# Performance work log

Hardware: AMD Instinct MI355X
Metric: run time of the kernel (lower is better)

Reference implementation:

```python
import jax, jax.numpy as jnp
import numpy as np

N_POINTS = 10000
N_SHAPES = 100
N_RAYS = 4096
SH_COEFFS = 16  # (sh_degree+1)^2, degree 3


def sh_basis(d):
    """Degree-3 real SH basis. d: [B,3] normalized dirs -> [B,16]."""
    x, y, z = d[:, 0], d[:, 1], d[:, 2]
    one = jnp.ones_like(x)
    return jnp.stack([
        0.282095 * one,
        0.488603 * y, 0.488603 * z, 0.488603 * x,
        1.092548 * x * y, 1.092548 * y * z, 0.315392 * (3.0 * z * z - 1.0),
        1.092548 * x * z, 0.546274 * (x * x - y * y),
        0.590044 * y * (3.0 * x * x - y * y), 2.890611 * x * y * z,
        0.457046 * y * (5.0 * z * z - 1.0), 0.373176 * z * (5.0 * z * z - 3.0),
        0.457046 * x * (5.0 * z * z - 1.0), 1.445306 * z * (x * x - y * y),
        0.590044 * x * (x * x - 3.0 * y * y),
    ], axis=-1)


def setup_inputs() -> dict:
    key = jax.random.key(0)
    ks = jax.random.split(key, 7)
    return {
        "rays_o": jax.random.normal(ks[0], (N_RAYS, 3), jnp.float32),
        "rays_d": jax.random.normal(ks[1], (N_RAYS, 3), jnp.float32),
        "positions": jax.random.normal(ks[2], (N_POINTS, 3), jnp.float32),
        "shape_indices": jax.random.randint(ks[3], (N_POINTS,), 0, N_SHAPES, jnp.int32),
        "log_delta": jax.random.normal(ks[4], (N_SHAPES,), jnp.float32) * 0.1 - 1.0,
        "log_sigma": jax.random.normal(ks[5], (N_SHAPES,), jnp.float32) * 0.1,
        "raw_opacity": jax.random.uniform(ks[6], (N_POINTS,), jnp.float32, -0.1, 0.1),
        "sh_coeffs": jax.random.normal(jax.random.fold_in(key, 7), (N_POINTS, SH_COEFFS, 3), jnp.float32) * 0.1,
    }


def reference(rays_o, rays_d, positions, shape_indices, log_delta, log_sigma, raw_opacity, sh_coeffs):
    # normalize view directions (F.normalize)
    d_norm = rays_d / jnp.linalg.norm(rays_d, axis=-1, keepdims=True)

    opacity = jax.nn.sigmoid(raw_opacity)           # [N]
    point_delta = jnp.exp(log_delta)[shape_indices]  # [N]
    point_sigma = jnp.exp(log_sigma)[shape_indices]  # [N]

    # SH shading: colors [N, B, 3]
    sh = sh_basis(d_norm)                            # [B, 16]
    colors = jax.nn.sigmoid(jnp.einsum('nkc,bk->nbc', sh_coeffs, sh))

    # per point / per ray geometry
    rel = positions[:, None, :] - rays_o[None, :, :]   # [N, B, 3]
    dist = jnp.linalg.norm(rel, axis=2)                # [N, B]
    dirs = rel / (dist[..., None] + 1e-8)              # [N, B, 3]
    dot = jnp.sum(dirs * d_norm[None, :, :], axis=2)   # [N, B]

    contrib = (jnp.exp(-point_delta[:, None] * (1.0 - dot) ** 2)
               * point_sigma[:, None] * opacity[:, None] / (dist + 1e-6))  # [N, B]
    total = jnp.sum(contrib, axis=0, keepdims=True)
    w = contrib / (total + 1e-8)                       # [N, B]

    rgb = jnp.sum(colors * w[..., None], axis=0)       # [B, 3]
    depth = jnp.sum(dist * w, axis=0)[:, None]         # [B, 1]
    opac = jnp.broadcast_to(jnp.mean(opacity), (rgb.shape[0],))
    return rgb, depth, opac
```

## Files before the change

### kernel.cpp

```cpp
#include <hip/hip_runtime.h>
#include <hip/hip_bf16.h>

#define NPTS    10000
#define NRAYS   4096
#define PTILES  640
#define RTILES  256
#define RGROUPS 64
#define PCHUNKS 16
#define TPC     (PTILES / PCHUNKS)
#define ABLK    64
#define BBLK    160
#define LOG2E   1.44269504f

typedef float f4  __attribute__((ext_vector_type(4)));
typedef short s8v __attribute__((ext_vector_type(8)));

__device__ s8v   g_A[RTILES * 4 * 64];
__device__ s8v   g_B[PTILES * 7 * 64];
__device__ float g_acc[NRAYS * 5];
__device__ float g_oppart[BBLK];

__device__ __forceinline__ float fast_rcp(float x)  { return __builtin_amdgcn_rcpf(x); }
__device__ __forceinline__ float fast_exp2(float x) { return __builtin_amdgcn_exp2f(x); }
__device__ __forceinline__ float fast_sigmoid(float x) { return fast_rcp(1.0f + fast_exp2(-x * LOG2E)); }

__device__ __forceinline__ unsigned short bf16r(float x) {
    __hip_bfloat16 h = __float2bfloat16(x);
    return *reinterpret_cast<unsigned short*>(&h);
}
__device__ __forceinline__ float bf16f(unsigned short u) {
    return __uint_as_float((unsigned)u << 16);
}
__device__ __forceinline__ float bfhi(float x) { return bf16f(bf16r(x)); }

__device__ __forceinline__ s8v pk8(float a, float b, float c, float d,
                                   float e, float f, float g, float h) {
    s8v r;
    r[0] = (short)bf16r(a); r[1] = (short)bf16r(b);
    r[2] = (short)bf16r(c); r[3] = (short)bf16r(d);
    r[4] = (short)bf16r(e); r[5] = (short)bf16r(f);
    r[6] = (short)bf16r(g); r[7] = (short)bf16r(h);
    return r;
}

template <int CTRL>
__device__ __forceinline__ float dpp_step(float x) {
    return x + __int_as_float(
        __builtin_amdgcn_update_dpp(0, __float_as_int(x), CTRL, 0xf, 0xf, true));
}
__device__ __forceinline__ float rowsum15(float x) {
    x = dpp_step<0x111>(x);
    x = dpp_step<0x112>(x);
    x = dpp_step<0x114>(x);
    x = dpp_step<0x118>(x);
    return x;
}

__global__ __launch_bounds__(256) void setup(const float* __restrict__ ro,
                                             const float* __restrict__ rd,
                                             const float* __restrict__ pos,
                                             const int*   __restrict__ sidx,
                                             const float* __restrict__ log_delta,
                                             const float* __restrict__ log_sigma,
                                             const float* __restrict__ raw_op,
                                             const float* __restrict__ shc) {
    s8v zero8 = pk8(0, 0, 0, 0, 0, 0, 0, 0);
    if (blockIdx.x < ABLK) {
        int t = blockIdx.x * 256 + threadIdx.x;
        int rt = t >> 6, lane = t & 63, quad = lane >> 4;
        int r = rt * 16 + (lane & 15);
        if (quad == 0) {
            float* a = g_acc + (size_t)r * 5;
            a[0] = a[1] = a[2] = a[3] = a[4] = 0.0f;
        }
        float ox = ro[r * 3 + 0], oy = ro[r * 3 + 1], oz = ro[r * 3 + 2];
        float rdx = rd[r * 3 + 0], rdy = rd[r * 3 + 1], rdz = rd[r * 3 + 2];
        float inv = __builtin_amdgcn_rsqf(rdx * rdx + rdy * rdy + rdz * rdz);
        float x = rdx * inv, y = rdy * inv, z = rdz * inv;
        float oo = ox * ox + oy * oy + oz * oz;
        float od = ox * x + oy * y + oz * z;
        float ohx = bfhi(ox), olx = ox - ohx;
        float ohy = bfhi(oy), oly = oy - ohy;
        float ohz = bfhi(oz), olz = oz - ohz;
        float dhx = bfhi(x),  dlx = x - dhx;
        float dhy = bfhi(y),  dly = y - dhy;
        float dhz = bfhi(z),  dlz = z - dhz;
        float ooh = bfhi(oo), ool = oo - ooh;
        float odh = bfhi(od), odl = od - odh;
        float zz = z * z, xx = x * x, yy = y * y;
        float sh[16];
        sh[0]  = LOG2E * 0.282095f;
        sh[1]  = LOG2E * 0.488603f * y;
        sh[2]  = LOG2E * 0.488603f * z;
        sh[3]  = LOG2E * 0.488603f * x;
        sh[4]  = LOG2E * 1.092548f * x * y;
        sh[5]  = LOG2E * 1.092548f * y * z;
        sh[6]  = LOG2E * 0.315392f * (3.0f * zz - 1.0f);
        sh[7]  = LOG2E * 1.092548f * x * z;
        sh[8]  = LOG2E * 0.546274f * (xx - yy);
        sh[9]  = LOG2E * 0.590044f * y * (3.0f * xx - yy);
        sh[10] = LOG2E * 2.890611f * x * y * z;
        sh[11] = LOG2E * 0.457046f * y * (5.0f * zz - 1.0f);
        sh[12] = LOG2E * 0.373176f * z * (5.0f * zz - 3.0f);
        sh[13] = LOG2E * 0.457046f * x * (5.0f * zz - 1.0f);
        sh[14] = LOG2E * 1.445306f * z * (xx - yy);
        sh[15] = LOG2E * 0.590044f * x * (xx - 3.0f * yy);

        s8v A0 = quad == 0 ? pk8(1, 1, ooh, ool, ohx, ohy, ohz, ohx)
               : quad == 1 ? pk8(ohy, ohz, olx, oly, olz, 0, 0, 0) : zero8;
        s8v A1 = quad == 0 ? pk8(dhx, dhy, dhz, dhx, dhy, dhz, dlx, dly)
               : quad == 1 ? pk8(dlz, odh, odl, 0, 0, 0, 0, 0) : zero8;
        s8v A2 = quad == 0 ? pk8(sh[0], sh[1], sh[2], sh[3], sh[4], sh[5], sh[6], sh[7])
               : quad == 1 ? pk8(sh[8], sh[9], sh[10], sh[11], sh[12], sh[13], sh[14], sh[15]) : zero8;
        s8v A3 = quad == 0 ? pk8(1, 1, 0, 0, 0, 0, 0, 0) : zero8;
        s8v* pa = g_A + (size_t)rt * 4 * 64 + lane;
        pa[0 * 64] = A0; pa[1 * 64] = A1; pa[2 * 64] = A2; pa[3 * 64] = A3;
    } else {
        int bb = blockIdx.x - ABLK;
        int t  = bb * 256 + threadIdx.x;
        int pt = t >> 6, lane = t & 63, quad = lane >> 4;
        int n  = pt * 16 + (lane & 15);
        float px, py, pz, w1, L0, op = 0.0f;
        float C0[16], C1[16], C2[16];
        if (n < NPTS) {
            px = pos[n * 3 + 0]; py = pos[n * 3 + 1]; pz = pos[n * 3 + 2];
            int s = sidx[n];
            op = fast_sigmoid(raw_op[n]);
            w1 = -__expf(log_delta[s]) * LOG2E;
            float w0 = __expf(log_sigma[s]) * op;
            L0 = __log2f(w0);
            const float* c = shc + (size_t)n * 48;
#pragma unroll
            for (int k = 0; k < 16; ++k) {
                C0[k] = c[k * 3 + 0]; C1[k] = c[k * 3 + 1]; C2[k] = c[k * 3 + 2];
            }
        } else {
            px = py = pz = 1e3f; w1 = 0.0f; L0 = -100.0f;
#pragma unroll
            for (int k = 0; k < 16; ++k) { C0[k] = 0; C1[k] = 0; C2[k] = 0; }
        }
        float pp  = px * px + py * py + pz * pz;
        float phx = bfhi(px), plx = px - phx;
        float phy = bfhi(py), ply = py - phy;
        float phz = bfhi(pz), plz = pz - phz;
        float pph = bfhi(pp), ppl = pp - pph;
        float w1h = bfhi(w1), w1l = w1 - w1h;
        float L0h = bfhi(L0), L0l = L0 - L0h;

        s8v B0 = quad == 0 ? pk8(pph, ppl, 1, 1, -2 * phx, -2 * phy, -2 * phz, -2 * plx)
               : quad == 1 ? pk8(-2 * ply, -2 * plz, -2 * phx, -2 * phy, -2 * phz, 0, 0, 0) : zero8;
        s8v B1 = quad == 0 ? pk8(phx, phy, phz, plx, ply, plz, phx, phy)
               : quad == 1 ? pk8(phz, -1, -1, 0, 0, 0, 0, 0) : zero8;
        s8v B2 = quad == 0 ? pk8(C0[0], C0[1], C0[2], C0[3], C0[4], C0[5], C0[6], C0[7])
               : quad == 1 ? pk8(C0[8], C0[9], C0[10], C0[11], C0[12], C0[13], C0[14], C0[15]) : zero8;
        s8v B3 = quad == 0 ? pk8(C1[0], C1[1], C1[2], C1[3], C1[4], C1[5], C1[6], C1[7])
               : quad == 1 ? pk8(C1[8], C1[9], C1[10], C1[11], C1[12], C1[13], C1[14], C1[15]) : zero8;
        s8v B4 = quad == 0 ? pk8(C2[0], C2[1], C2[2], C2[3], C2[4], C2[5], C2[6], C2[7])
               : quad == 1 ? pk8(C2[8], C2[9], C2[10], C2[11], C2[12], C2[13], C2[14], C2[15]) : zero8;
        s8v B5 = quad == 0 ? pk8(w1h, w1l, 0, 0, 0, 0, 0, 0) : zero8;
        s8v B6 = quad == 0 ? pk8(L0h, L0l, 0, 0, 0, 0, 0, 0) : zero8;
        s8v* pb = g_B + (size_t)pt * 7 * 64 + lane;
        pb[0 * 64] = B0; pb[1 * 64] = B1; pb[2 * 64] = B2; pb[3 * 64] = B3;
        pb[4 * 64] = B4; pb[5 * 64] = B5; pb[6 * 64] = B6;

        __shared__ float blk;
        if (threadIdx.x == 0) blk = 0.0f;
        __syncthreads();
        float v = (quad == 0) ? op : 0.0f;
#pragma unroll
        for (int off = 32; off > 0; off >>= 1) v += __shfl_down(v, off, 64);
        if ((threadIdx.x & 63) == 0) atomicAdd(&blk, v);
        __syncthreads();
        if (threadIdx.x == 0) g_oppart[bb] = blk;
    }
}

__global__ __launch_bounds__(256, 3) void nerf_main() {
    int rg = blockIdx.x & (RGROUPS - 1);
    int pc = blockIdx.x / RGROUPS;
    int wv = threadIdx.x >> 6, lane = threadIdx.x & 63;
    int rt = rg * 4 + wv;

    const s8v* pa = g_A + (size_t)rt * 4 * 64 + lane;
    s8v a0 = pa[0 * 64], a1 = pa[1 * 64], a2 = pa[2 * 64], a3 = pa[3 * 64];
    f4 z = {0.0f, 0.0f, 0.0f, 0.0f};

    float acc[5][4];
#pragma unroll
    for (int v = 0; v < 5; ++v)
#pragma unroll
        for (int i = 0; i < 4; ++i) acc[v][i] = 0.0f;

    const s8v* pb = g_B + (size_t)(pc * TPC) * 7 * 64 + lane;
#pragma unroll 1
    for (int ti = 0; ti < TPC; ++ti, pb += 7 * 64) {
        s8v b0 = pb[0 * 64], b1 = pb[1 * 64], b2 = pb[2 * 64], b3 = pb[3 * 64];
        s8v b4 = pb[4 * 64], b5 = pb[5 * 64], b6 = pb[6 * 64];
        f4 c0 = __builtin_amdgcn_mfma_f32_16x16x32_bf16(a0, b0, z, 0, 0, 0);
        f4 c1 = __builtin_amdgcn_mfma_f32_16x16x32_bf16(a1, b1, z, 0, 0, 0);
        f4 c2 = __builtin_amdgcn_mfma_f32_16x16x32_bf16(a2, b2, z, 0, 0, 0);
        f4 c3 = __builtin_amdgcn_mfma_f32_16x16x32_bf16(a2, b3, z, 0, 0, 0);
        f4 c4 = __builtin_amdgcn_mfma_f32_16x16x32_bf16(a2, b4, z, 0, 0, 0);
        f4 c5 = __builtin_amdgcn_mfma_f32_16x16x32_bf16(a3, b5, z, 0, 0, 0);
        f4 c6 = __builtin_amdgcn_mfma_f32_16x16x32_bf16(a3, b6, z, 0, 0, 0);
#pragma unroll
        for (int i = 0; i < 4; ++i) {
            float d2  = c0[i], pd = c1[i];
            float inv = __builtin_amdgcn_rsqf(d2);
            float t   = 1.0f - pd * inv;
            float arg = fmaf(c5[i] * t, t, c6[i]);
            float contrib = fast_exp2(arg) * inv;
            float dist = d2 * inv;
            float e0 = 1.0f + fast_exp2(-c2[i]);
            float e1 = 1.0f + fast_exp2(-c3[i]);
            float e2 = 1.0f + fast_exp2(-c4[i]);
            float P  = e0 * e1, Pa = P * e2;
            float CI = contrib * fast_rcp(Pa);
            acc[0][i] = fmaf(CI, e1 * e2, acc[0][i]);
            acc[1][i] = fmaf(CI, e0 * e2, acc[1][i]);
            acc[2][i] = fmaf(CI, P, acc[2][i]);
            acc[3][i] = fmaf(dist, contrib, acc[3][i]);
            acc[4][i] += contrib;
        }
    }

#pragma unroll
    for (int v = 0; v < 5; ++v)
#pragma unroll
        for (int i = 0; i < 4; ++i) acc[v][i] = rowsum15(acc[v][i]);
    if ((lane & 15) == 15) {
        int quad = lane >> 4;
#pragma unroll
        for (int i = 0; i < 4; ++i) {
            float* ac = g_acc + (size_t)(rt * 16 + quad * 4 + i) * 5;
            atomicAdd(ac + 0, acc[0][i]);
            atomicAdd(ac + 1, acc[1][i]);
            atomicAdd(ac + 2, acc[2][i]);
            atomicAdd(ac + 3, acc[3][i]);
            atomicAdd(ac + 4, acc[4][i]);
        }
    }
}

__global__ void finalize(float* __restrict__ out) {
    int r = blockIdx.x * blockDim.x + threadIdx.x;
    if (r >= NRAYS) return;
    float opv = 0.0f;
    for (int i = 0; i < BBLK; ++i) opv += g_oppart[i];
    const float* a = g_acc + (size_t)r * 5;
    float inv = fast_rcp(a[4] + 1e-8f);
    out[r * 3 + 0]     = a[0] * inv;
    out[r * 3 + 1]     = a[1] * inv;
    out[r * 3 + 2]     = a[2] * inv;
    out[NRAYS * 3 + r] = a[3] * inv;
    out[NRAYS * 4 + r] = opv * (1.0f / NPTS);
}

extern "C" void kernel_launch(void* const* d_in, const int* in_sizes, int n_in,
                              void* d_out, int out_size, void* d_ws, size_t ws_size,
                              hipStream_t stream) {
    const float* rays_o    = (const float*)d_in[0];
    const float* rays_d    = (const float*)d_in[1];
    const float* positions = (const float*)d_in[2];
    const int*   sidx      = (const int*)d_in[3];
    const float* log_delta = (const float*)d_in[4];
    const float* log_sigma = (const float*)d_in[5];
    const float* raw_op    = (const float*)d_in[6];
    const float* shc       = (const float*)d_in[7];

    setup<<<ABLK + BBLK, 256, 0, stream>>>(
        rays_o, rays_d, positions, sidx, log_delta, log_sigma, raw_op, shc);
    nerf_main<<<RGROUPS * PCHUNKS, 256, 0, stream>>>();
    finalize<<<NRAYS / 256, 256, 0, stream>>>((float*)d_out);
}
```

Baseline: 129.3 us.

## Process two ray tiles per wave and double-buffer point-tile loads

Each wave now handles two ray tiles, so every point-tile B fragment loaded from global memory is reused by two sets of MFMAs, halving B traffic per unit of work. Point tiles are prefetched into a second register buffer while the current one is computed, with asm barriers that keep the compiler from sinking the loads. The grid is reshaped (32 ray blocks by 32 point chunks) to keep the block count the same. The g_B array gains one padding tile so the final prefetch stays in bounds. The cost is roughly double the accumulator and fragment registers, which may hurt occupancy under the 3-blocks-per-SM launch bound.

```diff
diff --git a/kernel.cpp b/kernel.cpp
--- a/kernel.cpp
+++ b/kernel.cpp
@@ -5,8 +5,8 @@
 #define NRAYS   4096
 #define PTILES  640
 #define RTILES  256
-#define RGROUPS 64
-#define PCHUNKS 16
+#define RBLK    32
+#define PCHUNKS 32
 #define TPC     (PTILES / PCHUNKS)
 #define ABLK    64
 #define BBLK    160
@@ -16,7 +16,7 @@
 typedef short s8v __attribute__((ext_vector_type(8)));
 
 __device__ s8v   g_A[RTILES * 4 * 64];
-__device__ s8v   g_B[PTILES * 7 * 64];
+__device__ s8v   g_B[(PTILES + 1) * 7 * 64];
 __device__ float g_acc[NRAYS * 5];
 __device__ float g_oppart[BBLK];
 
@@ -175,70 +175,100 @@
     }
 }
 
+#define COMPUTE(B) {                                                          \
+    _Pragma("unroll")                                                         \
+    for (int rt = 0; rt < 2; ++rt) {                                          \
+        f4 c0 = __builtin_amdgcn_mfma_f32_16x16x32_bf16(a[rt][0], B[0], z, 0, 0, 0); \
+        f4 c1 = __builtin_amdgcn_mfma_f32_16x16x32_bf16(a[rt][1], B[1], z, 0, 0, 0); \
+        f4 c2 = __builtin_amdgcn_mfma_f32_16x16x32_bf16(a[rt][2], B[2], z, 0, 0, 0); \
+        f4 c3 = __builtin_amdgcn_mfma_f32_16x16x32_bf16(a[rt][2], B[3], z, 0, 0, 0); \
+        f4 c4 = __builtin_amdgcn_mfma_f32_16x16x32_bf16(a[rt][2], B[4], z, 0, 0, 0); \
+        f4 c5 = __builtin_amdgcn_mfma_f32_16x16x32_bf16(a[rt][3], B[5], z, 0, 0, 0); \
+        f4 c6 = __builtin_amdgcn_mfma_f32_16x16x32_bf16(a[rt][3], B[6], z, 0, 0, 0); \
+        _Pragma("unroll")                                                     \
+        for (int i = 0; i < 4; ++i) {                                         \
+            float d2  = c0[i], pd = c1[i];                                    \
+            float inv = __builtin_amdgcn_rsqf(d2);                            \
+            float t   = 1.0f - pd * inv;                                      \
+            float arg = fmaf(c5[i] * t, t, c6[i]);                            \
+            float contrib = fast_exp2(arg) * inv;                             \
+            float e0 = 1.0f + fast_exp2(-c2[i]);                              \
+            float e1 = 1.0f + fast_exp2(-c3[i]);                              \
+            float e2 = 1.0f + fast_exp2(-c4[i]);                              \
+            float P  = e0 * e1, Pa = P * e2;                                  \
+            float CI = contrib * fast_rcp(Pa);                                \
+            acc[rt][0][i] = fmaf(CI, e1 * e2, acc[rt][0][i]);                 \
+            acc[rt][1][i] = fmaf(CI, e0 * e2, acc[rt][1][i]);                 \
+            acc[rt][2][i] = fmaf(CI, P, acc[rt][2][i]);                       \
+            acc[rt][3][i] = fmaf(d2 * inv, contrib, acc[rt][3][i]);           \
+            acc[rt][4][i] += contrib;                                         \
+        }                                                                     \
+    }}
+
 __global__ __launch_bounds__(256, 3) void nerf_main() {
-    int rg = blockIdx.x & (RGROUPS - 1);
-    int pc = blockIdx.x / RGROUPS;
+    int rg = blockIdx.x & (RBLK - 1);
+    int pc = blockIdx.x / RBLK;
     int wv = threadIdx.x >> 6, lane = threadIdx.x & 63;
-    int rt = rg * 4 + wv;
-
-    const s8v* pa = g_A + (size_t)rt * 4 * 64 + lane;
-    s8v a0 = pa[0 * 64], a1 = pa[1 * 64], a2 = pa[2 * 64], a3 = pa[3 * 64];
+    int rt0 = rg * 8 + wv * 2;
+
+    s8v a[2][4];
+#pragma unroll
+    for (int rt = 0; rt < 2; ++rt) {
+        const s8v* pa = g_A + (size_t)(rt0 + rt) * 4 * 64 + lane;
+#pragma unroll
+        for (int f = 0; f < 4; ++f) a[rt][f] = pa[f * 64];
+    }
     f4 z = {0.0f, 0.0f, 0.0f, 0.0f};
 
-    float acc[5][4];
-#pragma unroll
-    for (int v = 0; v < 5; ++v)
-#pragma unroll
-        for (int i = 0; i < 4; ++i) acc[v][i] = 0.0f;
+    float acc[2][5][4];
+#pragma unroll
+    for (int rt = 0; rt < 2; ++rt)
+#pragma unroll
+        for (int v = 0; v < 5; ++v)
+#pragma unroll
+            for (int i = 0; i < 4; ++i) acc[rt][v][i] = 0.0f;
 
     const s8v* pb = g_B + (size_t)(pc * TPC) * 7 * 64 + lane;
+    s8v BQ0[7], BQ1[7];
+#pragma unroll
+    for (int f = 0; f < 7; ++f) BQ0[f] = pb[f * 64];
+    pb += 7 * 64;
+
 #pragma unroll 1
-    for (int ti = 0; ti < TPC; ++ti, pb += 7 * 64) {
-        s8v b0 = pb[0 * 64], b1 = pb[1 * 64], b2 = pb[2 * 64], b3 = pb[3 * 64];
-        s8v b4 = pb[4 * 64], b5 = pb[5 * 64], b6 = pb[6 * 64];
-        f4 c0 = __builtin_amdgcn_mfma_f32_16x16x32_bf16(a0, b0, z, 0, 0, 0);
-        f4 c1 = __builtin_amdgcn_mfma_f32_16x16x32_bf16(a1, b1, z, 0, 0, 0);
-        f4 c2 = __builtin_amdgcn_mfma_f32_16x16x32_bf16(a2, b2, z, 0, 0, 0);
-        f4 c3 = __builtin_amdgcn_mfma_f32_16x16x32_bf16(a2, b3, z, 0, 0, 0);
-        f4 c4 = __builtin_amdgcn_mfma_f32_16x16x32_bf16(a2, b4, z, 0, 0, 0);
-        f4 c5 = __builtin_amdgcn_mfma_f32_16x16x32_bf16(a3, b5, z, 0, 0, 0);
-        f4 c6 = __builtin_amdgcn_mfma_f32_16x16x32_bf16(a3, b6, z, 0, 0, 0);
-#pragma unroll
-        for (int i = 0; i < 4; ++i) {
-            float d2  = c0[i], pd = c1[i];
-            float inv = __builtin_amdgcn_rsqf(d2);
-            float t   = 1.0f - pd * inv;
-            float arg = fmaf(c5[i] * t, t, c6[i]);
-            float contrib = fast_exp2(arg) * inv;
-            float dist = d2 * inv;
-            float e0 = 1.0f + fast_exp2(-c2[i]);
-            float e1 = 1.0f + fast_exp2(-c3[i]);
-            float e2 = 1.0f + fast_exp2(-c4[i]);
-            float P  = e0 * e1, Pa = P * e2;
-            float CI = contrib * fast_rcp(Pa);
-            acc[0][i] = fmaf(CI, e1 * e2, acc[0][i]);
-            acc[1][i] = fmaf(CI, e0 * e2, acc[1][i]);
-            acc[2][i] = fmaf(CI, P, acc[2][i]);
-            acc[3][i] = fmaf(dist, contrib, acc[3][i]);
-            acc[4][i] += contrib;
-        }
+    for (int ti = 0; ti < TPC; ti += 2) {
+#pragma unroll
+        for (int f = 0; f < 7; ++f) BQ1[f] = pb[f * 64];
+        pb += 7 * 64;
+#pragma unroll
+        for (int f = 0; f < 7; ++f) asm volatile("" : "+v"(BQ1[f]));
+        COMPUTE(BQ0)
+#pragma unroll
+        for (int f = 0; f < 7; ++f) BQ0[f] = pb[f * 64];
+        pb += 7 * 64;
+#pragma unroll
+        for (int f = 0; f < 7; ++f) asm volatile("" : "+v"(BQ0[f]));
+        COMPUTE(BQ1)
     }
 
 #pragma unroll
-    for (int v = 0; v < 5; ++v)
-#pragma unroll
-        for (int i = 0; i < 4; ++i) acc[v][i] = rowsum15(acc[v][i]);
+    for (int rt = 0; rt < 2; ++rt)
+#pragma unroll
+        for (int v = 0; v < 5; ++v)
+#pragma unroll
+            for (int i = 0; i < 4; ++i) acc[rt][v][i] = rowsum15(acc[rt][v][i]);
     if ((lane & 15) == 15) {
         int quad = lane >> 4;
 #pragma unroll
-        for (int i = 0; i < 4; ++i) {
-            float* ac = g_acc + (size_t)(rt * 16 + quad * 4 + i) * 5;
-            atomicAdd(ac + 0, acc[0][i]);
-            atomicAdd(ac + 1, acc[1][i]);
-            atomicAdd(ac + 2, acc[2][i]);
-            atomicAdd(ac + 3, acc[3][i]);
-            atomicAdd(ac + 4, acc[4][i]);
-        }
+        for (int rt = 0; rt < 2; ++rt)
+#pragma unroll
+            for (int i = 0; i < 4; ++i) {
+                float* ac = g_acc + (size_t)((rt0 + rt) * 16 + quad * 4 + i) * 5;
+                atomicAdd(ac + 0, acc[rt][0][i]);
+                atomicAdd(ac + 1, acc[rt][1][i]);
+                atomicAdd(ac + 2, acc[rt][2][i]);
+                atomicAdd(ac + 3, acc[rt][3][i]);
+                atomicAdd(ac + 4, acc[rt][4][i]);
+            }
     }
 }
 
@@ -270,6 +300,6 @@
 
     setup<<<ABLK + BBLK, 256, 0, stream>>>(
         rays_o, rays_d, positions, sidx, log_delta, log_sigma, raw_op, shc);
-    nerf_main<<<RGROUPS * PCHUNKS, 256, 0, stream>>>();
+    nerf_main<<<RBLK * PCHUNKS, 256, 0, stream>>>();
     finalize<<<NRAYS / 256, 256, 0, stream>>>((float*)d_out);
 }
```

Measured after the change: 151.6 us. 1.17x slower.
